# Kernel tuning notes

Hardware: AMD Instinct MI355X
Metric: run time of the kernel (lower is better)

Reference implementation:

```python
import jax, jax.numpy as jnp
import numpy as np


def _fps_indices(xyz, num_points):
    """Furthest point sampling. xyz: [B, N, 3] -> indices [B, num_points] (int32)."""
    B, N, _ = xyz.shape

    def step(carry, _):
        dist, farthest = carry                                   # dist: [B, N], farthest: [B]
        centroid = jnp.take_along_axis(xyz, farthest[:, None, None], axis=1)  # [B, 1, 3]
        d = jnp.sum((xyz - centroid) ** 2, axis=-1)              # [B, N]
        dist = jnp.minimum(dist, d)
        nxt = jnp.argmax(dist, axis=-1).astype(jnp.int32)        # [B]
        return (dist, nxt), farthest

    init = (jnp.full((B, N), jnp.inf, dtype=xyz.dtype),
            jnp.zeros((B,), dtype=jnp.int32))                    # convention: start at index 0
    _, idxs = jax.lax.scan(step, init, None, length=num_points)  # [num_points, B]
    return idxs.T                                                # [B, num_points]


def setup_inputs() -> dict:
    key = jax.random.key(0)
    B, C, N = 16, 3, 131072
    points = jax.random.normal(key, (B, C, N), dtype=jnp.float32)
    return {"points": points, "num_points": 2048}


def reference(points, num_points):
    # points: [B, 3, N] channels-first, as in the torch module
    xyz = jnp.transpose(points, (0, 2, 1))                       # [B, N, 3]
    idx = _fps_indices(xyz, num_points)                          # [B, num_points]
    # fps_gather_by_index: gather along the point dim of the channels-first tensor
    new_points = jnp.take_along_axis(points, idx[:, None, :], axis=2)  # [B, 3, num_points]
    return new_points
```

## Files before the change

kernel.cpp:

```cpp
#include <hip/hip_runtime.h>
#include <stdint.h>


#define NBATCH    16
#define NPTS      131072
#define SUBBLOCKS 16
#define NTHREADS  1024
#define CHUNK     8192
#define HALF      4096

typedef unsigned long long u64;

__device__ __forceinline__ u64 umax64(u64 a, u64 b) { return a > b ? a : b; }

__global__ __launch_bounds__(NTHREADS, 4)
void fps_kernel(const float* __restrict__ points,
                float* __restrict__ out,
                u64* __restrict__ slots, int M)
{
  __shared__ u64 wkeys[NTHREADS / 64];
  __shared__ u64 winner_s;

  const int bid   = blockIdx.x;
  const int xcd   = bid & 7;
  const int ord   = bid >> 3;
  const int batch = xcd * 2 + (ord >> 4);
  const int sub   = ord & 15;
  const int tid   = threadIdx.x;
  const int wave  = tid >> 6;
  const int lane  = tid & 63;

  const float* __restrict__ px = points + (size_t)batch * 3 * NPTS;
  const float* __restrict__ py = px + NPTS;
  const float* __restrict__ pz = px + 2 * NPTS;
  float* outb = out + (size_t)batch * 3 * M;
  u64* bslots = slots + (size_t)batch * 2 * SUBBLOCKS;

  const int cbase = sub * CHUNK;
  const int g0 = cbase + (tid << 2);
  const int g1 = g0 + HALF;

  float4 A0 = *(const float4*)(px + g0);
  float4 B0 = *(const float4*)(py + g0);
  float4 C0 = *(const float4*)(pz + g0);
  float4 A1 = *(const float4*)(px + g1);
  float4 B1 = *(const float4*)(py + g1);
  float4 C1 = *(const float4*)(pz + g1);
  float x0=A0.x, x1=A0.y, x2=A0.z, x3=A0.w, x4=A1.x, x5=A1.y, x6=A1.z, x7=A1.w;
  float y0=B0.x, y1=B0.y, y2=B0.z, y3=B0.w, y4=B1.x, y5=B1.y, y6=B1.z, y7=B1.w;
  float z0=C0.x, z1=C0.y, z2=C0.z, z3=C0.w, z4=C1.x, z5=C1.y, z6=C1.z, z7=C1.w;
  asm volatile("" :
    "+v"(x0),"+v"(x1),"+v"(x2),"+v"(x3),"+v"(x4),"+v"(x5),"+v"(x6),"+v"(x7),
    "+v"(y0),"+v"(y1),"+v"(y2),"+v"(y3),"+v"(y4),"+v"(y5),"+v"(y6),"+v"(y7),
    "+v"(z0),"+v"(z1),"+v"(z2),"+v"(z3),"+v"(z4),"+v"(z5),"+v"(z6),"+v"(z7));

  float d0, d1, d2, d3, d4, d5, d6, d7;
  d0 = d1 = d2 = d3 = d4 = d5 = d6 = d7 = __builtin_inff();

  if (sub == 0 && tid == 0) {
    outb[0]     = px[0];
    outb[M]     = py[0];
    outb[2 * M] = pz[0];
  }

  int sel = 0;
  for (int t = 1; t < M; ++t) {
    float cx = px[sel], cy = py[sel], cz = pz[sel];

    float best = -1.0f;
    int bidx = 0;
#define STEP(XX, YY, ZZ, DREG, IDX) { \
    float dx = __fsub_rn((XX), cx); \
    float dy = __fsub_rn((YY), cy); \
    float dz = __fsub_rn((ZZ), cz); \
    float dd = __builtin_fmaf(dz, dz, __builtin_fmaf(dy, dy, __fmul_rn(dx, dx))); \
    DREG = DREG < dd ? DREG : dd; \
    if (DREG > best) { best = DREG; bidx = (IDX); } }
    STEP(x0, y0, z0, d0, g0 + 0)
    STEP(x1, y1, z1, d1, g0 + 1)
    STEP(x2, y2, z2, d2, g0 + 2)
    STEP(x3, y3, z3, d3, g0 + 3)
    STEP(x4, y4, z4, d4, g1 + 0)
    STEP(x5, y5, z5, d5, g1 + 1)
    STEP(x6, y6, z6, d6, g1 + 2)
    STEP(x7, y7, z7, d7, g1 + 3)

    u64 key = ((u64)__float_as_uint(best) << 17) | (u64)((NPTS - 1) - bidx);

#pragma unroll
    for (int m = 32; m >= 1; m >>= 1) {
      u64 o = __shfl_xor(key, m, 64);
      key = umax64(key, o);
    }
    if (lane == 0) wkeys[wave] = key;
    __syncthreads();

    if (wave == 0) {
      u64 k = wkeys[lane & 15];
#pragma unroll
      for (int m = 8; m >= 1; m >>= 1) {
        u64 o = __shfl_xor(k, m, 64);
        k = umax64(k, o);
      }
      u64* par = bslots + (size_t)(t & 1) * SUBBLOCKS;
      if (lane == 0) {
        __hip_atomic_store(par + sub, ((u64)t << 49) | k,
                           __ATOMIC_RELAXED, __HIP_MEMORY_SCOPE_AGENT);
      }
      const u64* pp = par + (lane & 15);
      u64 v;
      for (;;) {
        v = __hip_atomic_load(pp, __ATOMIC_RELAXED, __HIP_MEMORY_SCOPE_AGENT);
        if (__ballot((unsigned)(v >> 49) == (unsigned)t) == ~0ull) break;
      }
#pragma unroll
      for (int m = 8; m >= 1; m >>= 1) {
        u64 o = __shfl_xor(v, m, 64);
        v = umax64(v, o);
      }
      if (lane == 0) winner_s = v;
    }
    __syncthreads();

    sel = (NPTS - 1) - (int)(winner_s & 0x1FFFF);

    if (sub == 0 && tid == 0) {
      outb[t]         = px[sel];
      outb[M + t]     = py[sel];
      outb[2 * M + t] = pz[sel];
    }
  }
}

extern "C" void kernel_launch(void* const* d_in, const int* in_sizes, int n_in,
                              void* d_out, int out_size, void* d_ws, size_t ws_size,
                              hipStream_t stream) {
  (void)in_sizes; (void)n_in; (void)ws_size;
  const float* points = (const float*)d_in[0];
  float* out = (float*)d_out;
  u64* slots = (u64*)d_ws;
  const int M = out_size / (NBATCH * 3);

  hipMemsetAsync(d_ws, 0, (size_t)NBATCH * 2 * SUBBLOCKS * sizeof(u64), stream);

  hipLaunchKernelGGL(fps_kernel, dim3(NBATCH * SUBBLOCKS), dim3(NTHREADS), 0,
                     stream, points, out, slots, M);
}
```

Before: 4.125 ms.

## Replace per-iteration __syncthreads with LDS atomics and per-step mailbox spin

Both __syncthreads barriers in the FPS loop are removed. Each wave now combines its key into a per-iteration LDS slot with atomicMax and marks itself done with atomicOr, and the last wave to arrive publishes the block result to global memory. Wave 0 polls the cross-block slots with a software-pipelined double load, then writes the winner into a per-iteration LDS mailbox that the other waves spin on. This is meant to cut barrier latency on the serial critical path, at the cost of LDS spinning and atomic contention, plus about 28KB more LDS, which may lower occupancy.

Measured after the change: 7.274 ms. +76.3%, slower.

```diff
diff --git a/kernel.cpp b/kernel.cpp
--- a/kernel.cpp
+++ b/kernel.cpp
@@ -6,8 +6,10 @@
 #define NPTS      131072
 #define SUBBLOCKS 16
 #define NTHREADS  1024
+#define NWAVES    16
 #define CHUNK     8192
 #define HALF      4096
+#define MMAX      2048
 
 typedef unsigned long long u64;
 
@@ -18,8 +20,9 @@
                 float* __restrict__ out,
                 u64* __restrict__ slots, int M)
 {
-  __shared__ u64 wkeys[NTHREADS / 64];
-  __shared__ u64 winner_s;
+  __shared__ u64      Lkey[MMAX];
+  __shared__ unsigned Lmask[MMAX];
+  __shared__ u64      Wwin[MMAX];
 
   const int bid   = blockIdx.x;
   const int xcd   = bid & 7;
@@ -35,6 +38,10 @@
   const float* __restrict__ pz = px + 2 * NPTS;
   float* outb = out + (size_t)batch * 3 * M;
   u64* bslots = slots + (size_t)batch * 2 * SUBBLOCKS;
+
+  for (int i = tid; i < MMAX; i += NTHREADS) {
+    Lkey[i] = 0; Lmask[i] = 0; Wwin[i] = 0;
+  }
 
   const int cbase = sub * CHUNK;
   const int g0 = cbase + (tid << 2);
@@ -57,16 +64,12 @@
   float d0, d1, d2, d3, d4, d5, d6, d7;
   d0 = d1 = d2 = d3 = d4 = d5 = d6 = d7 = __builtin_inff();
 
-  if (sub == 0 && tid == 0) {
-    outb[0]     = px[0];
-    outb[M]     = py[0];
-    outb[2 * M] = pz[0];
-  }
+  float cx = px[0], cy = py[0], cz = pz[0];
+  if (sub == 0 && tid == 0) { outb[0] = cx; outb[M] = cy; outb[2 * M] = cz; }
 
-  int sel = 0;
+  __syncthreads();
+
   for (int t = 1; t < M; ++t) {
-    float cx = px[sel], cy = py[sel], cz = pz[sel];
-
     float best = -1.0f;
     int bidx = 0;
 #define STEP(XX, YY, ZZ, DREG, IDX) { \
@@ -92,42 +95,56 @@
       u64 o = __shfl_xor(key, m, 64);
       key = umax64(key, o);
     }
-    if (lane == 0) wkeys[wave] = key;
-    __syncthreads();
 
-    if (wave == 0) {
-      u64 k = wkeys[lane & 15];
-#pragma unroll
-      for (int m = 8; m >= 1; m >>= 1) {
-        u64 o = __shfl_xor(k, m, 64);
-        k = umax64(k, o);
-      }
-      u64* par = bslots + (size_t)(t & 1) * SUBBLOCKS;
-      if (lane == 0) {
-        __hip_atomic_store(par + sub, ((u64)t << 49) | k,
+    u64* par = bslots + (size_t)(t & 1) * SUBBLOCKS;
+
+    if (lane == 0) {
+      atomicMax((u64*)&Lkey[t], key);
+      unsigned old = atomicOr(&Lmask[t], 1u << wave);
+      if ((old | (1u << wave)) == 0xFFFFu) {
+        u64 fk = __hip_atomic_load(&Lkey[t], __ATOMIC_RELAXED,
+                                   __HIP_MEMORY_SCOPE_WORKGROUP);
+        __hip_atomic_store(par + sub, ((u64)t << 49) | fk,
                            __ATOMIC_RELAXED, __HIP_MEMORY_SCOPE_AGENT);
       }
+    }
+
+    u64 wk;
+    if (wave == 0) {
       const u64* pp = par + (lane & 15);
+      u64 va = __hip_atomic_load(pp, __ATOMIC_RELAXED, __HIP_MEMORY_SCOPE_AGENT);
+      u64 vb = __hip_atomic_load(pp, __ATOMIC_RELAXED, __HIP_MEMORY_SCOPE_AGENT);
       u64 v;
       for (;;) {
-        v = __hip_atomic_load(pp, __ATOMIC_RELAXED, __HIP_MEMORY_SCOPE_AGENT);
-        if (__ballot((unsigned)(v >> 49) == (unsigned)t) == ~0ull) break;
+        if (__ballot((unsigned)(va >> 49) == (unsigned)t) == ~0ull) { v = va; break; }
+        va = vb;
+        vb = __hip_atomic_load(pp, __ATOMIC_RELAXED, __HIP_MEMORY_SCOPE_AGENT);
       }
 #pragma unroll
       for (int m = 8; m >= 1; m >>= 1) {
         u64 o = __shfl_xor(v, m, 64);
         v = umax64(v, o);
       }
-      if (lane == 0) winner_s = v;
+      if (lane == 0) {
+        __hip_atomic_store(&Wwin[t], v, __ATOMIC_RELAXED,
+                           __HIP_MEMORY_SCOPE_WORKGROUP);
+      }
+      wk = v;
+    } else {
+      do {
+        wk = __hip_atomic_load(&Wwin[t], __ATOMIC_RELAXED,
+                               __HIP_MEMORY_SCOPE_WORKGROUP);
+      } while ((unsigned)(wk >> 49) != (unsigned)t);
     }
-    __syncthreads();
 
-    sel = (NPTS - 1) - (int)(winner_s & 0x1FFFF);
+    int ssel = __builtin_amdgcn_readfirstlane(
+                 (int)(NPTS - 1) - (int)(wk & 0x1FFFF));
+    cx = px[ssel]; cy = py[ssel]; cz = pz[ssel];
 
     if (sub == 0 && tid == 0) {
-      outb[t]         = px[sel];
-      outb[M + t]     = py[sel];
-      outb[2 * M + t] = pz[sel];
+      outb[t]         = cx;
+      outb[M + t]     = cy;
+      outb[2 * M + t] = cz;
     }
   }
 }
```

## Add sc0 dwordx2 fast-path slot exchange with fallback to atomic slots

Applied to the files above, without the earlier changes.

Each block now publishes its local winner twice. One copy goes to a new slot array as a packed, tagged 64-bit pair written with sc0 stores, and the other goes to the existing agent-scope atomic slot. Waiting blocks poll the new slots with sc0 loads and check the 8-bit tags on both 32-bit halves, falling back to the atomic slots every fourth round. The aim is to cut the latency of the inter-block barrier/reduction that runs on every FPS iteration. The centroid coordinate load is also moved to right after the winner is chosen, and the output store reuses those values. The sc0-only coherence and the short tags add risk of stale or torn reads between XCDs, and the fallback path exists to guard against that.

New measurement: 4.800 ms. 1.16x slower.

```diff
diff --git a/kernel.cpp b/kernel.cpp
--- a/kernel.cpp
+++ b/kernel.cpp
@@ -10,13 +10,16 @@
 #define HALF      4096
 
 typedef unsigned long long u64;
+typedef unsigned int u32;
 
 __device__ __forceinline__ u64 umax64(u64 a, u64 b) { return a > b ? a : b; }
 
 __global__ __launch_bounds__(NTHREADS, 4)
 void fps_kernel(const float* __restrict__ points,
                 float* __restrict__ out,
-                u64* __restrict__ slots, int M)
+                u64* __restrict__ dslots,
+                u32* __restrict__ lslots,
+                int M)
 {
   __shared__ u64 wkeys[NTHREADS / 64];
   __shared__ u64 winner_s;
@@ -34,7 +37,8 @@
   const float* __restrict__ py = px + NPTS;
   const float* __restrict__ pz = px + 2 * NPTS;
   float* outb = out + (size_t)batch * 3 * M;
-  u64* bslots = slots + (size_t)batch * 2 * SUBBLOCKS;
+  u64* dbase = dslots + (size_t)batch * 2 * SUBBLOCKS;
+  u32* lbase = lslots + (size_t)batch * 64;
 
   const int cbase = sub * CHUNK;
   const int g0 = cbase + (tid << 2);
@@ -54,19 +58,14 @@
     "+v"(y0),"+v"(y1),"+v"(y2),"+v"(y3),"+v"(y4),"+v"(y5),"+v"(y6),"+v"(y7),
     "+v"(z0),"+v"(z1),"+v"(z2),"+v"(z3),"+v"(z4),"+v"(z5),"+v"(z6),"+v"(z7));
 
-  float d0, d1, d2, d3, d4, d5, d6, d7;
-  d0 = d1 = d2 = d3 = d4 = d5 = d6 = d7 = __builtin_inff();
+  float d0r, d1r, d2r, d3r, d4r, d5r, d6r, d7r;
+  d0r = d1r = d2r = d3r = d4r = d5r = d6r = d7r = __builtin_inff();
 
-  if (sub == 0 && tid == 0) {
-    outb[0]     = px[0];
-    outb[M]     = py[0];
-    outb[2 * M] = pz[0];
-  }
+  float cx = px[0], cy = py[0], cz = pz[0];
+  if (sub == 0 && tid == 0) { outb[0] = cx; outb[M] = cy; outb[2 * M] = cz; }
 
   int sel = 0;
   for (int t = 1; t < M; ++t) {
-    float cx = px[sel], cy = py[sel], cz = pz[sel];
-
     float best = -1.0f;
     int bidx = 0;
 #define STEP(XX, YY, ZZ, DREG, IDX) { \
@@ -76,14 +75,14 @@
     float dd = __builtin_fmaf(dz, dz, __builtin_fmaf(dy, dy, __fmul_rn(dx, dx))); \
     DREG = DREG < dd ? DREG : dd; \
     if (DREG > best) { best = DREG; bidx = (IDX); } }
-    STEP(x0, y0, z0, d0, g0 + 0)
-    STEP(x1, y1, z1, d1, g0 + 1)
-    STEP(x2, y2, z2, d2, g0 + 2)
-    STEP(x3, y3, z3, d3, g0 + 3)
-    STEP(x4, y4, z4, d4, g1 + 0)
-    STEP(x5, y5, z5, d5, g1 + 1)
-    STEP(x6, y6, z6, d6, g1 + 2)
-    STEP(x7, y7, z7, d7, g1 + 3)
+    STEP(x0, y0, z0, d0r, g0 + 0)
+    STEP(x1, y1, z1, d1r, g0 + 1)
+    STEP(x2, y2, z2, d2r, g0 + 2)
+    STEP(x3, y3, z3, d3r, g0 + 3)
+    STEP(x4, y4, z4, d4r, g1 + 0)
+    STEP(x5, y5, z5, d5r, g1 + 1)
+    STEP(x6, y6, z6, d6r, g1 + 2)
+    STEP(x7, y7, z7, d7r, g1 + 3)
 
     u64 key = ((u64)__float_as_uint(best) << 17) | (u64)((NPTS - 1) - bidx);
 
@@ -102,32 +101,73 @@
         u64 o = __shfl_xor(k, m, 64);
         k = umax64(k, o);
       }
-      u64* par = bslots + (size_t)(t & 1) * SUBBLOCKS;
+      const u32 tag8 = (u32)t & 255u;
+      u64* dpar = dbase + (size_t)(t & 1) * SUBBLOCKS;
+      u32* lpar = lbase + (size_t)(t & 1) * 32;
+
       if (lane == 0) {
-        __hip_atomic_store(par + sub, ((u64)t << 49) | k,
+        u32 D = (u32)(k >> 17);
+        int  g = (int)(NPTS - 1) - (int)(k & 0x1FFFF);
+        u32  L = (u32)(8191 - (g - cbase));
+        u32 w0 = (tag8 << 24) | (D >> 8);
+        u32 w1 = (tag8 << 24) | ((D & 0xFFu) << 16) | (L << 3);
+        u64 both = ((u64)w1 << 32) | w0;
+        const u32* lp = lpar + sub * 2;
+        asm volatile("global_store_dwordx2 %0, %1, off sc0"
+                     :: "v"(lp), "v"(both) : "memory");
+        __hip_atomic_store(dpar + sub, ((u64)t << 49) | k,
                            __ATOMIC_RELAXED, __HIP_MEMORY_SCOPE_AGENT);
       }
-      const u64* pp = par + (lane & 15);
-      u64 v;
+
+      const u32* lpp = lpar + (lane & 15) * 2;
+      const u64* dpp = dpar + (lane & 15);
+      u64 win;
+      int round = 0;
       for (;;) {
-        v = __hip_atomic_load(pp, __ATOMIC_RELAXED, __HIP_MEMORY_SCOPE_AGENT);
-        if (__ballot((unsigned)(v >> 49) == (unsigned)t) == ~0ull) break;
+        u64 raw;
+        asm volatile("global_load_dwordx2 %0, %1, off sc0\n\t"
+                     "s_waitcnt vmcnt(0)"
+                     : "=v"(raw) : "v"(lpp) : "memory");
+        u32 a0 = (u32)raw, a1 = (u32)(raw >> 32);
+        bool ok = ((a0 >> 24) == tag8) & ((a1 >> 24) == tag8);
+        if (__ballot(ok) == ~0ull) {
+          u32 D = ((a0 & 0xFFFFFFu) << 8) | ((a1 >> 16) & 0xFFu);
+          int  L = (int)((a1 >> 3) & 0x1FFFu);
+          int  g = (lane & 15) * CHUNK + (8191 - L);
+          u64 kk = ((u64)D << 17) | (u64)((NPTS - 1) - g);
+#pragma unroll
+          for (int m = 8; m >= 1; m >>= 1) {
+            u64 o = __shfl_xor(kk, m, 64);
+            kk = umax64(kk, o);
+          }
+          win = ((u64)t << 49) | kk;
+          break;
+        }
+        if ((++round & 3) == 0) {
+          u64 v = __hip_atomic_load(dpp, __ATOMIC_RELAXED,
+                                    __HIP_MEMORY_SCOPE_AGENT);
+          if (__ballot((unsigned)(v >> 49) == (unsigned)t) == ~0ull) {
+#pragma unroll
+            for (int m = 8; m >= 1; m >>= 1) {
+              u64 o = __shfl_xor(v, m, 64);
+              v = umax64(v, o);
+            }
+            win = v;
+            break;
+          }
+        }
       }
-#pragma unroll
-      for (int m = 8; m >= 1; m >>= 1) {
-        u64 o = __shfl_xor(v, m, 64);
-        v = umax64(v, o);
-      }
-      if (lane == 0) winner_s = v;
+      if (lane == 0) winner_s = win;
     }
     __syncthreads();
 
     sel = (NPTS - 1) - (int)(winner_s & 0x1FFFF);
+    cx = px[sel]; cy = py[sel]; cz = pz[sel];
 
     if (sub == 0 && tid == 0) {
-      outb[t]         = px[sel];
-      outb[M + t]     = py[sel];
-      outb[2 * M + t] = pz[sel];
+      outb[t]         = cx;
+      outb[M + t]     = cy;
+      outb[2 * M + t] = cz;
     }
   }
 }
@@ -138,11 +178,12 @@
   (void)in_sizes; (void)n_in; (void)ws_size;
   const float* points = (const float*)d_in[0];
   float* out = (float*)d_out;
-  u64* slots = (u64*)d_ws;
+  u64* dslots = (u64*)d_ws;
+  u32* lslots = (u32*)((char*)d_ws + 4096);
   const int M = out_size / (NBATCH * 3);
 
-  hipMemsetAsync(d_ws, 0, (size_t)NBATCH * 2 * SUBBLOCKS * sizeof(u64), stream);
+  hipMemsetAsync(d_ws, 0, 8192, stream);
 
   hipLaunchKernelGGL(fps_kernel, dim3(NBATCH * SUBBLOCKS), dim3(NTHREADS), 0,
-                     stream, points, out, slots, M);
+                     stream, points, out, dslots, lslots, M);
 }
```
